# Kernel optimization log

Measured on AMD Instinct MI355X. Metric: run time of the kernel, lower is better.

Reference implementation:

```python
import jax, jax.numpy as jnp
import numpy as np

B, T, C = 2, 2048, 1024
H = 16
D = C // H  # head_dim = 64


def setup_inputs() -> dict:
    key = jax.random.key(0)
    ks = jax.random.split(key, 9)
    s = 0.02
    return {
        "x": jax.random.normal(ks[0], (B, T, C), dtype=jnp.float32),
        "Wq": jax.random.normal(ks[1], (C, C), dtype=jnp.float32) * s,
        "bq": jax.random.normal(ks[2], (C,), dtype=jnp.float32) * s,
        "Wk": jax.random.normal(ks[3], (C, C), dtype=jnp.float32) * s,
        "bk": jax.random.normal(ks[4], (C,), dtype=jnp.float32) * s,
        "Wv": jax.random.normal(ks[5], (C, C), dtype=jnp.float32) * s,
        "bv": jax.random.normal(ks[6], (C,), dtype=jnp.float32) * s,
        "Wo": jax.random.normal(ks[7], (C, C), dtype=jnp.float32) * s,
        "bo": jax.random.normal(ks[8], (C,), dtype=jnp.float32) * s,
    }


def reference(x, Wq, bq, Wk, bk, Wv, bv, Wo, bo):
    b, t, c = x.shape
    h, d = H, c // H
    # torch nn.Linear: y = x @ W.T + b
    q = (x @ Wq.T + bq).reshape(b, t, h, d).transpose(0, 2, 1, 3)  # [B,H,T,D]
    k = (x @ Wk.T + bk).reshape(b, t, h, d).transpose(0, 2, 1, 3)
    v = (x @ Wv.T + bv).reshape(b, t, h, d).transpose(0, 2, 1, 3)

    scores = jnp.einsum("bhqd,bhkd->bhqk", q, k) / jnp.sqrt(jnp.float32(d))
    causal = jnp.tril(jnp.ones((t, t), dtype=bool))  # [T,T]
    scores = jnp.where(causal[None, None, :, :], scores, -jnp.inf)
    attn = jax.nn.softmax(scores, axis=-1)  # [B,H,T,T]

    out = jnp.einsum("bhqk,bhkd->bhqd", attn, v)  # [B,H,T,D]
    out = out.transpose(0, 2, 1, 3).reshape(b, t, c)
    out = out @ Wo.T + bo
    return out
```

## Files before the change

### kernel.cpp

```cpp
#include <hip/hip_runtime.h>
#include <hip/hip_bf16.h>

using u16 = unsigned short;
using u32 = unsigned int;
using short8  = __attribute__((ext_vector_type(8))) short;
using short4v = __attribute__((ext_vector_type(4))) short;
using floatx4 = __attribute__((ext_vector_type(4))) float;

#define TT 2048
#define CC 1024
#define HH 16
#define DD 64
#define BBATCH 2
#define MM (BBATCH*TT)

#define QSCALE 0.18033688011112042f

__device__ __forceinline__ u16 f2bf(float f) {
    u32 u = __float_as_uint(f);
    u += 0x7fffu + ((u >> 16) & 1u);
    return (u16)(u >> 16);
}
__device__ __forceinline__ float bf2f(u16 s) {
    return __uint_as_float(((u32)s) << 16);
}
__device__ __forceinline__ float bpermf(float v, int srclane) {
    return __int_as_float(__builtin_amdgcn_ds_bpermute(srclane * 4, __float_as_int(v)));
}
__device__ __forceinline__ void gll16(const u16* g, u16* l) {
    __builtin_amdgcn_global_load_lds((const __attribute__((address_space(1))) void*)g,
                                     (__attribute__((address_space(3))) void*)l, 16, 0, 0);
}

__global__ __launch_bounds__(256) void cast_all(const float* __restrict__ x,
    const float* __restrict__ Wq, const float* __restrict__ Wk,
    const float* __restrict__ Wv, const float* __restrict__ Wo,
    u16* __restrict__ xb, u16* __restrict__ wqb, u16* __restrict__ wkb,
    u16* __restrict__ wvb, u16* __restrict__ wob)
{
    int i = blockIdx.x * 256 + threadIdx.x;
    const float* src; u16* dst; int off;
    if (i < 1048576) { src = x; dst = xb; off = i; }
    else {
        int j = i - 1048576;
        int s = j >> 18;
        off = j & 262143;
        src = (s == 0) ? Wq : (s == 1) ? Wk : (s == 2) ? Wv : Wo;
        dst = (s == 0) ? wqb : (s == 1) ? wkb : (s == 2) ? wvb : wob;
    }
    float4 v = ((const float4*)src)[off];
    u16 r[4];
    r[0] = f2bf(v.x); r[1] = f2bf(v.y); r[2] = f2bf(v.z); r[3] = f2bf(v.w);
    ((ushort4*)dst)[off] = *(ushort4*)r;
}

__global__ __launch_bounds__(256) void transpose_v(const u16* __restrict__ v, u16* __restrict__ vt) {
    __shared__ u16 tile[64][72];
    int bh = blockIdx.y;
    int t0 = blockIdx.x * 64;
    int r = threadIdx.x >> 2;
    int c = (threadIdx.x & 3) * 16;
    const u16* src = v + ((size_t)bh * TT + t0 + r) * DD + c;
    *(uint4*)&tile[r][c]     = *(const uint4*)src;
    *(uint4*)&tile[r][c + 8] = *(const uint4*)(src + 8);
    __syncthreads();
    u16 tmp[16];
#pragma unroll
    for (int j = 0; j < 16; ++j) tmp[j] = tile[c + j][r];
    u16* dst = vt + ((size_t)bh * DD + r) * TT + t0 + c;
    *(uint4*)dst       = *(uint4*)&tmp[0];
    *(uint4*)(dst + 8) = *(uint4*)&tmp[8];
}

template <int OUT_MODE>
__device__ __forceinline__ void gemm_core(const u16* __restrict__ A, const u16* __restrict__ W,
                                          const float* __restrict__ bias, float outscale,
                                          void* __restrict__ outp)
{
    __shared__ u16 As[128*32];
    __shared__ u16 Bs[128*32];
    const int K = CC;
    int tid = threadIdx.x;
    int m0 = blockIdx.y * 128;
    int n0 = blockIdx.x * 128;
    int lane = tid & 63;
    int w  = tid >> 6;
    int wm = (w >> 1) * 64;
    int wn = (w & 1) * 64;
    int lm = lane & 15;
    int lq = lane >> 4;

    floatx4 acc[4][4];
#pragma unroll
    for (int i = 0; i < 4; ++i)
#pragma unroll
        for (int j = 0; j < 4; ++j)
            acc[i][j] = (floatx4){0.f, 0.f, 0.f, 0.f};

    const u16* ag = A + (size_t)(m0 + (tid >> 2)) * K + (tid & 3) * 8;
    const u16* wg = W + (size_t)(n0 + (tid >> 2)) * K + (tid & 3) * 8;
    u16* asl = As + tid * 8;
    u16* bsl = Bs + tid * 8;

    for (int k0 = 0; k0 < K; k0 += 32) {
        __syncthreads();
        gll16(ag + k0,           asl);
        gll16(ag + 64*K + k0,    asl + 2048);
        gll16(wg + k0,           bsl);
        gll16(wg + 64*K + k0,    bsl + 2048);
        __syncthreads();
        short8 af[4], bfr[4];
#pragma unroll
        for (int t = 0; t < 4; ++t) {
            af[t]  = *(const short8*)(As + (wm + t*16 + lm)*32 + lq*8);
            bfr[t] = *(const short8*)(Bs + (wn + t*16 + lm)*32 + lq*8);
        }
#pragma unroll
        for (int i = 0; i < 4; ++i)
#pragma unroll
            for (int j = 0; j < 4; ++j)
                acc[i][j] = __builtin_amdgcn_mfma_f32_16x16x32_bf16(af[i], bfr[j], acc[i][j], 0, 0, 0);
    }

#pragma unroll
    for (int j = 0; j < 4; ++j) {
        int col = n0 + wn + j*16 + lm;
        float bv = bias[col];
#pragma unroll
        for (int i = 0; i < 4; ++i) {
#pragma unroll
            for (int r = 0; r < 4; ++r) {
                int row = m0 + wm + i*16 + lq*4 + r;
                float val = (acc[i][j][r] + bv) * outscale;
                if (OUT_MODE == 0) {
                    int b_ = row >> 11, t_ = row & (TT-1);
                    int h_ = col >> 6,  d_ = col & 63;
                    ((u16*)outp)[(((size_t)(b_*HH + h_) * TT + t_) * DD) + d_] = f2bf(val);
                } else {
                    ((float*)outp)[(size_t)row * CC + col] = val;
                }
            }
        }
    }
}

__global__ __launch_bounds__(256, 2) void qkv_gemm(const u16* __restrict__ xb,
    const u16* __restrict__ wq, const u16* __restrict__ wk, const u16* __restrict__ wv,
    const float* __restrict__ bq, const float* __restrict__ bk, const float* __restrict__ bv,
    u16* __restrict__ q, u16* __restrict__ k, u16* __restrict__ v)
{
    int z = blockIdx.z;
    const u16* W = (z == 0) ? wq : (z == 1) ? wk : wv;
    const float* bias = (z == 0) ? bq : (z == 1) ? bk : bv;
    u16* outp = (z == 0) ? q : (z == 1) ? k : v;
    float scl = (z == 0) ? QSCALE : 1.0f;
    gemm_core<0>(xb, W, bias, scl, outp);
}

__global__ __launch_bounds__(256, 2) void o_gemm(const u16* __restrict__ a, const u16* __restrict__ w,
                                                 const float* __restrict__ bias, float* __restrict__ outp)
{
    gemm_core<1>(a, w, bias, 1.0f, outp);
}

__global__ __launch_bounds__(256, 2) void attn_mfma(const u16* __restrict__ qg, const u16* __restrict__ kg,
                                                    const u16* __restrict__ vtg, u16* __restrict__ attnb)
{
    __shared__ u16 Ks[64*72];
    __shared__ u16 Vs[64*72];

    int tid = threadIdx.x;
    int lane = tid & 63;
    int w = tid >> 6;
    int lm = lane & 15;
    int lq = lane >> 4;
    int qt = (int)(gridDim.x - 1) - (int)blockIdx.x;
    int bh = blockIdx.y;
    int b_ = bh >> 4, h_ = bh & 15;
    int q0 = qt * 128;

    const size_t basek  = (size_t)bh * TT * DD;
    const size_t basevt = (size_t)bh * DD * TT;

    short8 aq[2][2];
    {
        const u16* qbase = qg + basek + (size_t)(q0 + w*32 + lm) * DD + lq*8;
#pragma unroll
        for (int i = 0; i < 2; ++i)
#pragma unroll
            for (int ks = 0; ks < 2; ++ks)
                aq[i][ks] = *(const short8*)(qbase + i*16*DD + ks*32);
    }

    floatx4 oacc[2][4];
#pragma unroll
    for (int i = 0; i < 2; ++i)
#pragma unroll
        for (int j = 0; j < 4; ++j)
            oacc[i][j] = (floatx4){0.f, 0.f, 0.f, 0.f};
    float mrun[2] = {-3e38f, -3e38f};
    float lrun[2] = {0.f, 0.f};

    int srow = tid >> 2;
    int kb   = tid & 3;
    int p_   = kb >> 1, kb01 = kb & 1;
    const u16* ksrc = kg  + basek  + (size_t)srow * DD + kb*16;
    const u16* vsrc = vtg + basevt + (size_t)srow * TT + kb*16;
    u16* kdst = Ks + srow*72 + kb*16;
    u16* vdst = Vs + srow*72 + p_*32 + kb01*4;

    int nkt = 2*qt + 2;
    int wrowmax = q0 + w*32 + 31;

    for (int kt = 0; kt < nkt; ++kt) {
        uint4 k0v = *(const uint4*)(ksrc + (size_t)kt*64*DD);
        uint4 k1v = *(const uint4*)(ksrc + (size_t)kt*64*DD + 8);
        uint4 v0v = *(const uint4*)(vsrc + kt*64);
        uint4 v1v = *(const uint4*)(vsrc + kt*64 + 8);
        __syncthreads();
        *(uint4*)kdst       = k0v;
        *(uint4*)(kdst + 8) = k1v;
        *(uint2*)(vdst)      = make_uint2(v0v.x, v0v.y);
        *(uint2*)(vdst + 8)  = make_uint2(v0v.z, v0v.w);
        *(uint2*)(vdst + 16) = make_uint2(v1v.x, v1v.y);
        *(uint2*)(vdst + 24) = make_uint2(v1v.z, v1v.w);
        __syncthreads();

        if (kt*64 <= wrowmax) {
            floatx4 st[2][4];
#pragma unroll
            for (int i = 0; i < 2; ++i)
#pragma unroll
                for (int jn = 0; jn < 4; ++jn)
                    st[i][jn] = (floatx4){0.f, 0.f, 0.f, 0.f};
#pragma unroll
            for (int jn = 0; jn < 4; ++jn) {
                short8 kf0 = *(const short8*)&Ks[(jn*16 + lm)*72 + lq*8];
                short8 kf1 = *(const short8*)&Ks[(jn*16 + lm)*72 + 32 + lq*8];
#pragma unroll
                for (int i = 0; i < 2; ++i) {
                    st[i][jn] = __builtin_amdgcn_mfma_f32_16x16x32_bf16(kf0, aq[i][0], st[i][jn], 0, 0, 0);
                    st[i][jn] = __builtin_amdgcn_mfma_f32_16x16x32_bf16(kf1, aq[i][1], st[i][jn], 0, 0, 0);
                }
            }

            int kbase = kt*64;
            short4v ap[2][4];
#pragma unroll
            for (int i = 0; i < 2; ++i) {
                int qrow = q0 + w*32 + i*16 + lm;
                if (kbase + 63 > q0 + w*32 + i*16) {
#pragma unroll
                    for (int jn = 0; jn < 4; ++jn)
#pragma unroll
                        for (int r = 0; r < 4; ++r) {
                            int key = kbase + jn*16 + lq*4 + r;
                            if (key > qrow) st[i][jn][r] = -__builtin_inff();
                        }
                }
                float mx = st[i][0][0];
#pragma unroll
                for (int jn = 0; jn < 4; ++jn)
#pragma unroll
                    for (int r = 0; r < 4; ++r) mx = fmaxf(mx, st[i][jn][r]);
                mx = fmaxf(mx, __shfl_xor(mx, 16));
                mx = fmaxf(mx, __shfl_xor(mx, 32));
                float mold = mrun[i];
                float newm = fmaxf(mold, mx);
                mrun[i] = newm;
                float psum = 0.f;
#pragma unroll
                for (int jn = 0; jn < 4; ++jn)
#pragma unroll
                    for (int r = 0; r < 4; ++r) {
                        float pe = __builtin_amdgcn_exp2f(st[i][jn][r] - newm);
                        st[i][jn][r] = pe;
                        psum += pe;
                    }
                psum += __shfl_xor(psum, 16);
                psum += __shfl_xor(psum, 32);
                float alpha = __builtin_amdgcn_exp2f(mold - newm);
                lrun[i] = lrun[i]*alpha + psum;
#pragma unroll
                for (int jn = 0; jn < 4; ++jn) {
                    u32 lo = __builtin_amdgcn_perm(__float_as_uint(st[i][jn][1]),
                                                   __float_as_uint(st[i][jn][0]), 0x07060302u);
                    u32 hi = __builtin_amdgcn_perm(__float_as_uint(st[i][jn][3]),
                                                   __float_as_uint(st[i][jn][2]), 0x07060302u);
                    uint2 pk = make_uint2(lo, hi);
                    ap[i][jn] = __builtin_bit_cast(short4v, pk);
                }
                if (__ballot(newm != mold)) {
                    float ar[4];
#pragma unroll
                    for (int r = 0; r < 4; ++r) ar[r] = bpermf(alpha, lq*4 + r);
#pragma unroll
                    for (int jd = 0; jd < 4; ++jd)
#pragma unroll
                        for (int r = 0; r < 4; ++r) oacc[i][jd][r] *= ar[r];
                }
            }

#pragma unroll
            for (int p2 = 0; p2 < 2; ++p2) {
#pragma unroll
                for (int jd = 0; jd < 4; ++jd) {
                    short8 vb = *(const short8*)&Vs[(jd*16 + lm)*72 + p2*32 + lq*8];
                    short4v blo, bhi;
#pragma unroll
                    for (int j = 0; j < 4; ++j) { blo[j] = vb[j]; bhi[j] = vb[j+4]; }
#pragma unroll
                    for (int i = 0; i < 2; ++i) {
                        oacc[i][jd] = __builtin_amdgcn_mfma_f32_16x16x16bf16_1k(ap[i][2*p2],   blo, oacc[i][jd], 0, 0, 0);
                        oacc[i][jd] = __builtin_amdgcn_mfma_f32_16x16x16bf16_1k(ap[i][2*p2+1], bhi, oacc[i][jd], 0, 0, 0);
                    }
                }
            }
        }
    }

#pragma unroll
    for (int i = 0; i < 2; ++i) {
        float il[4];
#pragma unroll
        for (int r = 0; r < 4; ++r) il[r] = 1.f / bpermf(lrun[i], lq*4 + r);
#pragma unroll
        for (int r = 0; r < 4; ++r) {
            int qrow = q0 + w*32 + i*16 + lq*4 + r;
            u16* orow = attnb + ((size_t)(b_*TT + qrow)) * CC + h_*DD + lm;
#pragma unroll
            for (int jd = 0; jd < 4; ++jd)
                orow[jd*16] = f2bf(oacc[i][jd][r] * il[r]);
        }
    }
}

extern "C" void kernel_launch(void* const* d_in, const int* in_sizes, int n_in,
                              void* d_out, int out_size, void* d_ws, size_t ws_size,
                              hipStream_t stream)
{
    const float* x  = (const float*)d_in[0];
    const float* Wq = (const float*)d_in[1];
    const float* bq = (const float*)d_in[2];
    const float* Wk = (const float*)d_in[3];
    const float* bk = (const float*)d_in[4];
    const float* Wv = (const float*)d_in[5];
    const float* bv = (const float*)d_in[6];
    const float* Wo = (const float*)d_in[7];
    const float* bo = (const float*)d_in[8];
    float* out = (float*)d_out;

    char* ws = (char*)d_ws;
    u16* xb   = (u16*)(ws);
    u16* wqb  = (u16*)(ws + (size_t)( 8<<20));
    u16* wkb  = (u16*)(ws + (size_t)(10<<20));
    u16* wvb  = (u16*)(ws + (size_t)(12<<20));
    u16* wob  = (u16*)(ws + (size_t)(14<<20));
    u16* q    = (u16*)(ws + (size_t)(16<<20));
    u16* k    = (u16*)(ws + (size_t)(24<<20));
    u16* v    = (u16*)(ws + (size_t)(32<<20));
    u16* vt   = (u16*)(ws + (size_t)(40<<20));
    u16* attnb = xb;

    cast_all<<<dim3(8192), dim3(256), 0, stream>>>(x, Wq, Wk, Wv, Wo, xb, wqb, wkb, wvb, wob);

    dim3 gq(CC/128, MM/128, 3);
    qkv_gemm<<<gq, dim3(256), 0, stream>>>(xb, wqb, wkb, wvb, bq, bk, bv, q, k, v);

    transpose_v<<<dim3(TT/64, BBATCH*HH), dim3(256), 0, stream>>>(v, vt);

    attn_mfma<<<dim3(TT/128, BBATCH*HH), dim3(256), 0, stream>>>(q, k, vt, attnb);

    dim3 go(CC/128, MM/128);
    o_gemm<<<go, dim3(256), 0, stream>>>(attnb, wob, bo, out);
}
```

Measured before the change: 219.0 us.

## Shrink attention to 64-row query tiles and split O-projection into narrower tiles

The attention kernel now runs 128-thread blocks over 64 query rows, so twice as many blocks are launched and causal work is spread more evenly across CUs. K tiles are loaded straight into LDS with global-to-LDS loads into an unpadded layout, and the per-warp causal skip branch is removed. The O-projection GEMM is split out of the shared template with 128x64 tiles and a higher occupancy bound, doubling its block count. The cost is that each K/V tile now feeds fewer query rows, and the unpadded K layout may cause LDS bank conflicts.

```diff
diff --git a/kernel.cpp b/kernel.cpp
--- a/kernel.cpp
+++ b/kernel.cpp
@@ -72,14 +72,20 @@
     *(uint4*)(dst + 8) = *(uint4*)&tmp[8];
 }
 
-template <int OUT_MODE>
-__device__ __forceinline__ void gemm_core(const u16* __restrict__ A, const u16* __restrict__ W,
-                                          const float* __restrict__ bias, float outscale,
-                                          void* __restrict__ outp)
+__global__ __launch_bounds__(256, 2) void qkv_gemm(const u16* __restrict__ xb,
+    const u16* __restrict__ wq, const u16* __restrict__ wk, const u16* __restrict__ wv,
+    const float* __restrict__ bq, const float* __restrict__ bk, const float* __restrict__ bv,
+    u16* __restrict__ q, u16* __restrict__ k, u16* __restrict__ v)
 {
     __shared__ u16 As[128*32];
     __shared__ u16 Bs[128*32];
     const int K = CC;
+    int z = blockIdx.z;
+    const u16* W = (z == 0) ? wq : (z == 1) ? wk : wv;
+    const float* bias = (z == 0) ? bq : (z == 1) ? bk : bv;
+    u16* outp = (z == 0) ? q : (z == 1) ? k : v;
+    float outscale = (z == 0) ? QSCALE : 1.0f;
+
     int tid = threadIdx.x;
     int m0 = blockIdx.y * 128;
     int n0 = blockIdx.x * 128;
@@ -97,6 +103,70 @@
         for (int j = 0; j < 4; ++j)
             acc[i][j] = (floatx4){0.f, 0.f, 0.f, 0.f};
 
+    const u16* ag = xb + (size_t)(m0 + (tid >> 2)) * K + (tid & 3) * 8;
+    const u16* wg = W  + (size_t)(n0 + (tid >> 2)) * K + (tid & 3) * 8;
+    u16* asl = As + tid * 8;
+    u16* bsl = Bs + tid * 8;
+
+    for (int k0 = 0; k0 < K; k0 += 32) {
+        __syncthreads();
+        gll16(ag + k0,           asl);
+        gll16(ag + 64*K + k0,    asl + 2048);
+        gll16(wg + k0,           bsl);
+        gll16(wg + 64*K + k0,    bsl + 2048);
+        __syncthreads();
+        short8 af[4], bfr[4];
+#pragma unroll
+        for (int t = 0; t < 4; ++t) {
+            af[t]  = *(const short8*)(As + (wm + t*16 + lm)*32 + lq*8);
+            bfr[t] = *(const short8*)(Bs + (wn + t*16 + lm)*32 + lq*8);
+        }
+#pragma unroll
+        for (int i = 0; i < 4; ++i)
+#pragma unroll
+            for (int j = 0; j < 4; ++j)
+                acc[i][j] = __builtin_amdgcn_mfma_f32_16x16x32_bf16(af[i], bfr[j], acc[i][j], 0, 0, 0);
+    }
+
+#pragma unroll
+    for (int j = 0; j < 4; ++j) {
+        int col = n0 + wn + j*16 + lm;
+        float bv2 = bias[col];
+#pragma unroll
+        for (int i = 0; i < 4; ++i) {
+#pragma unroll
+            for (int r = 0; r < 4; ++r) {
+                int row = m0 + wm + i*16 + lq*4 + r;
+                float val = (acc[i][j][r] + bv2) * outscale;
+                int b_ = row >> 11, t_ = row & (TT-1);
+                int h_ = col >> 6,  d_ = col & 63;
+                outp[(((size_t)(b_*HH + h_) * TT + t_) * DD) + d_] = f2bf(val);
+            }
+        }
+    }
+}
+
+__global__ __launch_bounds__(256, 4) void o_gemm(const u16* __restrict__ A, const u16* __restrict__ W,
+                                                 const float* __restrict__ bias, float* __restrict__ outp)
+{
+    __shared__ u16 As[128*32];
+    __shared__ u16 Bs[64*32];
+    const int K = CC;
+    int tid = threadIdx.x;
+    int m0 = blockIdx.y * 128;
+    int n0 = blockIdx.x * 64;
+    int lane = tid & 63;
+    int w  = tid >> 6;
+    int lm = lane & 15;
+    int lq = lane >> 4;
+
+    floatx4 acc[2][4];
+#pragma unroll
+    for (int i = 0; i < 2; ++i)
+#pragma unroll
+        for (int j = 0; j < 4; ++j)
+            acc[i][j] = (floatx4){0.f, 0.f, 0.f, 0.f};
+
     const u16* ag = A + (size_t)(m0 + (tid >> 2)) * K + (tid & 3) * 8;
     const u16* wg = W + (size_t)(n0 + (tid >> 2)) * K + (tid & 3) * 8;
     u16* asl = As + tid * 8;
@@ -104,19 +174,19 @@
 
     for (int k0 = 0; k0 < K; k0 += 32) {
         __syncthreads();
-        gll16(ag + k0,           asl);
-        gll16(ag + 64*K + k0,    asl + 2048);
-        gll16(wg + k0,           bsl);
-        gll16(wg + 64*K + k0,    bsl + 2048);
-        __syncthreads();
-        short8 af[4], bfr[4];
-#pragma unroll
-        for (int t = 0; t < 4; ++t) {
-            af[t]  = *(const short8*)(As + (wm + t*16 + lm)*32 + lq*8);
-            bfr[t] = *(const short8*)(Bs + (wn + t*16 + lm)*32 + lq*8);
-        }
-#pragma unroll
-        for (int i = 0; i < 4; ++i)
+        gll16(ag + k0,        asl);
+        gll16(ag + 64*K + k0, asl + 2048);
+        gll16(wg + k0,        bsl);
+        __syncthreads();
+        short8 af[2], bfr[4];
+#pragma unroll
+        for (int i = 0; i < 2; ++i)
+            af[i] = *(const short8*)(As + (w*32 + i*16 + lm)*32 + lq*8);
+#pragma unroll
+        for (int j = 0; j < 4; ++j)
+            bfr[j] = *(const short8*)(Bs + (j*16 + lm)*32 + lq*8);
+#pragma unroll
+        for (int i = 0; i < 2; ++i)
 #pragma unroll
             for (int j = 0; j < 4; ++j)
                 acc[i][j] = __builtin_amdgcn_mfma_f32_16x16x32_bf16(af[i], bfr[j], acc[i][j], 0, 0, 0);
@@ -124,49 +194,23 @@
 
 #pragma unroll
     for (int j = 0; j < 4; ++j) {
-        int col = n0 + wn + j*16 + lm;
-        float bv = bias[col];
-#pragma unroll
-        for (int i = 0; i < 4; ++i) {
+        int col = n0 + j*16 + lm;
+        float bv2 = bias[col];
+#pragma unroll
+        for (int i = 0; i < 2; ++i) {
 #pragma unroll
             for (int r = 0; r < 4; ++r) {
-                int row = m0 + wm + i*16 + lq*4 + r;
-                float val = (acc[i][j][r] + bv) * outscale;
-                if (OUT_MODE == 0) {
-                    int b_ = row >> 11, t_ = row & (TT-1);
-                    int h_ = col >> 6,  d_ = col & 63;
-                    ((u16*)outp)[(((size_t)(b_*HH + h_) * TT + t_) * DD) + d_] = f2bf(val);
-                } else {
-                    ((float*)outp)[(size_t)row * CC + col] = val;
-                }
-            }
-        }
-    }
-}
-
-__global__ __launch_bounds__(256, 2) void qkv_gemm(const u16* __restrict__ xb,
-    const u16* __restrict__ wq, const u16* __restrict__ wk, const u16* __restrict__ wv,
-    const float* __restrict__ bq, const float* __restrict__ bk, const float* __restrict__ bv,
-    u16* __restrict__ q, u16* __restrict__ k, u16* __restrict__ v)
-{
-    int z = blockIdx.z;
-    const u16* W = (z == 0) ? wq : (z == 1) ? wk : wv;
-    const float* bias = (z == 0) ? bq : (z == 1) ? bk : bv;
-    u16* outp = (z == 0) ? q : (z == 1) ? k : v;
-    float scl = (z == 0) ? QSCALE : 1.0f;
-    gemm_core<0>(xb, W, bias, scl, outp);
-}
-
-__global__ __launch_bounds__(256, 2) void o_gemm(const u16* __restrict__ a, const u16* __restrict__ w,
-                                                 const float* __restrict__ bias, float* __restrict__ outp)
-{
-    gemm_core<1>(a, w, bias, 1.0f, outp);
-}
-
-__global__ __launch_bounds__(256, 2) void attn_mfma(const u16* __restrict__ qg, const u16* __restrict__ kg,
+                int row = m0 + w*32 + i*16 + lq*4 + r;
+                outp[(size_t)row * CC + col] = acc[i][j][r] + bv2;
+            }
+        }
+    }
+}
+
+__global__ __launch_bounds__(128, 2) void attn_mfma(const u16* __restrict__ qg, const u16* __restrict__ kg,
                                                     const u16* __restrict__ vtg, u16* __restrict__ attnb)
 {
-    __shared__ u16 Ks[64*72];
+    __shared__ u16 Ks[64*64];
     __shared__ u16 Vs[64*72];
 
     int tid = threadIdx.x;
@@ -174,10 +218,10 @@
     int w = tid >> 6;
     int lm = lane & 15;
     int lq = lane >> 4;
-    int qt = (int)(gridDim.x - 1) - (int)blockIdx.x;
+    int qt = 31 - (int)blockIdx.x;
     int bh = blockIdx.y;
     int b_ = bh >> 4, h_ = bh & 15;
-    int q0 = qt * 128;
+    int q0 = qt * 64;
 
     const size_t basek  = (size_t)bh * TT * DD;
     const size_t basevt = (size_t)bh * DD * TT;
@@ -201,119 +245,121 @@
     float mrun[2] = {-3e38f, -3e38f};
     float lrun[2] = {0.f, 0.f};
 
-    int srow = tid >> 2;
-    int kb   = tid & 3;
-    int p_   = kb >> 1, kb01 = kb & 1;
-    const u16* ksrc = kg  + basek  + (size_t)srow * DD + kb*16;
-    const u16* vsrc = vtg + basevt + (size_t)srow * TT + kb*16;
-    u16* kdst = Ks + srow*72 + kb*16;
-    u16* vdst = Vs + srow*72 + p_*32 + kb01*4;
-
-    int nkt = 2*qt + 2;
-    int wrowmax = q0 + w*32 + 31;
+    const u16* kgl = kg + basek + (size_t)(w*32 + (lane >> 3)) * DD + (lane & 7) * 8;
+    u16* kls = Ks + w*32*64 + lane*8;
+    int vrow = tid >> 1;
+    int kbv  = (tid & 1) * 2;
+    const u16* vsrc = vtg + basevt + (size_t)vrow * TT + kbv*16;
+    u16* vdst0 = Vs + vrow*72 + (kbv>>1)*32 + (kbv&1)*4;
+    u16* vdst1 = Vs + vrow*72 + ((kbv+1)>>1)*32 + ((kbv+1)&1)*4;
+
+    int nkt = qt + 1;
 
     for (int kt = 0; kt < nkt; ++kt) {
-        uint4 k0v = *(const uint4*)(ksrc + (size_t)kt*64*DD);
-        uint4 k1v = *(const uint4*)(ksrc + (size_t)kt*64*DD + 8);
-        uint4 v0v = *(const uint4*)(vsrc + kt*64);
-        uint4 v1v = *(const uint4*)(vsrc + kt*64 + 8);
-        __syncthreads();
-        *(uint4*)kdst       = k0v;
-        *(uint4*)(kdst + 8) = k1v;
-        *(uint2*)(vdst)      = make_uint2(v0v.x, v0v.y);
-        *(uint2*)(vdst + 8)  = make_uint2(v0v.z, v0v.w);
-        *(uint2*)(vdst + 16) = make_uint2(v1v.x, v1v.y);
-        *(uint2*)(vdst + 24) = make_uint2(v1v.z, v1v.w);
-        __syncthreads();
-
-        if (kt*64 <= wrowmax) {
-            floatx4 st[2][4];
-#pragma unroll
-            for (int i = 0; i < 2; ++i)
+        uint4 v0a = *(const uint4*)(vsrc + kt*64);
+        uint4 v0b = *(const uint4*)(vsrc + kt*64 + 8);
+        uint4 v1a = *(const uint4*)(vsrc + kt*64 + 16);
+        uint4 v1b = *(const uint4*)(vsrc + kt*64 + 24);
+        __syncthreads();
+#pragma unroll
+        for (int c = 0; c < 4; ++c)
+            gll16(kgl + (size_t)(kt*64 + c*8) * DD, kls + c*512);
+        *(uint2*)(vdst0)      = make_uint2(v0a.x, v0a.y);
+        *(uint2*)(vdst0 + 8)  = make_uint2(v0a.z, v0a.w);
+        *(uint2*)(vdst0 + 16) = make_uint2(v0b.x, v0b.y);
+        *(uint2*)(vdst0 + 24) = make_uint2(v0b.z, v0b.w);
+        *(uint2*)(vdst1)      = make_uint2(v1a.x, v1a.y);
+        *(uint2*)(vdst1 + 8)  = make_uint2(v1a.z, v1a.w);
+        *(uint2*)(vdst1 + 16) = make_uint2(v1b.x, v1b.y);
+        *(uint2*)(vdst1 + 24) = make_uint2(v1b.z, v1b.w);
+        __syncthreads();
+
+        floatx4 st[2][4];
+#pragma unroll
+        for (int i = 0; i < 2; ++i)
+#pragma unroll
+            for (int jn = 0; jn < 4; ++jn)
+                st[i][jn] = (floatx4){0.f, 0.f, 0.f, 0.f};
+#pragma unroll
+        for (int jn = 0; jn < 4; ++jn) {
+            short8 kf0 = *(const short8*)&Ks[(jn*16 + lm)*64 + lq*8];
+            short8 kf1 = *(const short8*)&Ks[(jn*16 + lm)*64 + 32 + lq*8];
+#pragma unroll
+            for (int i = 0; i < 2; ++i) {
+                st[i][jn] = __builtin_amdgcn_mfma_f32_16x16x32_bf16(kf0, aq[i][0], st[i][jn], 0, 0, 0);
+                st[i][jn] = __builtin_amdgcn_mfma_f32_16x16x32_bf16(kf1, aq[i][1], st[i][jn], 0, 0, 0);
+            }
+        }
+
+        int kbase = kt*64;
+        short4v ap[2][4];
+#pragma unroll
+        for (int i = 0; i < 2; ++i) {
+            int qrow = q0 + w*32 + i*16 + lm;
+            if (kbase + 63 > q0 + w*32 + i*16) {
 #pragma unroll
                 for (int jn = 0; jn < 4; ++jn)
-                    st[i][jn] = (floatx4){0.f, 0.f, 0.f, 0.f};
+#pragma unroll
+                    for (int r = 0; r < 4; ++r) {
+                        int key = kbase + jn*16 + lq*4 + r;
+                        if (key > qrow) st[i][jn][r] = -__builtin_inff();
+                    }
+            }
+            float mx = st[i][0][0];
+#pragma unroll
+            for (int jn = 0; jn < 4; ++jn)
+#pragma unroll
+                for (int r = 0; r < 4; ++r) mx = fmaxf(mx, st[i][jn][r]);
+            mx = fmaxf(mx, __shfl_xor(mx, 16));
+            mx = fmaxf(mx, __shfl_xor(mx, 32));
+            float mold = mrun[i];
+            float newm = fmaxf(mold, mx);
+            mrun[i] = newm;
+            float psum = 0.f;
+#pragma unroll
+            for (int jn = 0; jn < 4; ++jn)
+#pragma unroll
+                for (int r = 0; r < 4; ++r) {
+                    float pe = __builtin_amdgcn_exp2f(st[i][jn][r] - newm);
+                    st[i][jn][r] = pe;
+                    psum += pe;
+                }
+            psum += __shfl_xor(psum, 16);
+            psum += __shfl_xor(psum, 32);
+            float alpha = __builtin_amdgcn_exp2f(mold - newm);
+            lrun[i] = lrun[i]*alpha + psum;
 #pragma unroll
             for (int jn = 0; jn < 4; ++jn) {
-                short8 kf0 = *(const short8*)&Ks[(jn*16 + lm)*72 + lq*8];
-                short8 kf1 = *(const short8*)&Ks[(jn*16 + lm)*72 + 32 + lq*8];
+                u32 lo = __builtin_amdgcn_perm(__float_as_uint(st[i][jn][1]),
+                                               __float_as_uint(st[i][jn][0]), 0x07060302u);
+                u32 hi = __builtin_amdgcn_perm(__float_as_uint(st[i][jn][3]),
+                                               __float_as_uint(st[i][jn][2]), 0x07060302u);
+                uint2 pk = make_uint2(lo, hi);
+                ap[i][jn] = __builtin_bit_cast(short4v, pk);
+            }
+            if (__ballot(newm != mold)) {
+                float ar[4];
+#pragma unroll
+                for (int r = 0; r < 4; ++r) ar[r] = bpermf(alpha, lq*4 + r);
+#pragma unroll
+                for (int jd = 0; jd < 4; ++jd)
+#pragma unroll
+                    for (int r = 0; r < 4; ++r) oacc[i][jd][r] *= ar[r];
+            }
+        }
+
+#pragma unroll
+        for (int p2 = 0; p2 < 2; ++p2) {
+#pragma unroll
+            for (int jd = 0; jd < 4; ++jd) {
+                short8 vb = *(const short8*)&Vs[(jd*16 + lm)*72 + p2*32 + lq*8];
+                short4v blo, bhi;
+#pragma unroll
+                for (int j = 0; j < 4; ++j) { blo[j] = vb[j]; bhi[j] = vb[j+4]; }
 #pragma unroll
                 for (int i = 0; i < 2; ++i) {
-                    st[i][jn] = __builtin_amdgcn_mfma_f32_16x16x32_bf16(kf0, aq[i][0], st[i][jn], 0, 0, 0);
-                    st[i][jn] = __builtin_amdgcn_mfma_f32_16x16x32_bf16(kf1, aq[i][1], st[i][jn], 0, 0, 0);
-                }
-            }
-
-            int kbase = kt*64;
-            short4v ap[2][4];
-#pragma unroll
-            for (int i = 0; i < 2; ++i) {
-                int qrow = q0 + w*32 + i*16 + lm;
-                if (kbase + 63 > q0 + w*32 + i*16) {
-#pragma unroll
-                    for (int jn = 0; jn < 4; ++jn)
-#pragma unroll
-                        for (int r = 0; r < 4; ++r) {
-                            int key = kbase + jn*16 + lq*4 + r;
-                            if (key > qrow) st[i][jn][r] = -__builtin_inff();
-                        }
-                }
-                float mx = st[i][0][0];
-#pragma unroll
-                for (int jn = 0; jn < 4; ++jn)
-#pragma unroll
-                    for (int r = 0; r < 4; ++r) mx = fmaxf(mx, st[i][jn][r]);
-                mx = fmaxf(mx, __shfl_xor(mx, 16));
-                mx = fmaxf(mx, __shfl_xor(mx, 32));
-                float mold = mrun[i];
-                float newm = fmaxf(mold, mx);
-                mrun[i] = newm;
-                float psum = 0.f;
-#pragma unroll
-                for (int jn = 0; jn < 4; ++jn)
-#pragma unroll
-                    for (int r = 0; r < 4; ++r) {
-                        float pe = __builtin_amdgcn_exp2f(st[i][jn][r] - newm);
-                        st[i][jn][r] = pe;
-                        psum += pe;
-                    }
-                psum += __shfl_xor(psum, 16);
-                psum += __shfl_xor(psum, 32);
-                float alpha = __builtin_amdgcn_exp2f(mold - newm);
-                lrun[i] = lrun[i]*alpha + psum;
-#pragma unroll
-                for (int jn = 0; jn < 4; ++jn) {
-                    u32 lo = __builtin_amdgcn_perm(__float_as_uint(st[i][jn][1]),
-                                                   __float_as_uint(st[i][jn][0]), 0x07060302u);
-                    u32 hi = __builtin_amdgcn_perm(__float_as_uint(st[i][jn][3]),
-                                                   __float_as_uint(st[i][jn][2]), 0x07060302u);
-                    uint2 pk = make_uint2(lo, hi);
-                    ap[i][jn] = __builtin_bit_cast(short4v, pk);
-                }
-                if (__ballot(newm != mold)) {
-                    float ar[4];
-#pragma unroll
-                    for (int r = 0; r < 4; ++r) ar[r] = bpermf(alpha, lq*4 + r);
-#pragma unroll
-                    for (int jd = 0; jd < 4; ++jd)
-#pragma unroll
-                        for (int r = 0; r < 4; ++r) oacc[i][jd][r] *= ar[r];
-                }
-            }
-
-#pragma unroll
-            for (int p2 = 0; p2 < 2; ++p2) {
-#pragma unroll
-                for (int jd = 0; jd < 4; ++jd) {
-                    short8 vb = *(const short8*)&Vs[(jd*16 + lm)*72 + p2*32 + lq*8];
-                    short4v blo, bhi;
-#pragma unroll
-                    for (int j = 0; j < 4; ++j) { blo[j] = vb[j]; bhi[j] = vb[j+4]; }
-#pragma unroll
-                    for (int i = 0; i < 2; ++i) {
-                        oacc[i][jd] = __builtin_amdgcn_mfma_f32_16x16x16bf16_1k(ap[i][2*p2],   blo, oacc[i][jd], 0, 0, 0);
-                        oacc[i][jd] = __builtin_amdgcn_mfma_f32_16x16x16bf16_1k(ap[i][2*p2+1], bhi, oacc[i][jd], 0, 0, 0);
-                    }
+                    oacc[i][jd] = __builtin_amdgcn_mfma_f32_16x16x16bf16_1k(ap[i][2*p2],   blo, oacc[i][jd], 0, 0, 0);
+                    oacc[i][jd] = __builtin_amdgcn_mfma_f32_16x16x16bf16_1k(ap[i][2*p2+1], bhi, oacc[i][jd], 0, 0, 0);
                 }
             }
         }
@@ -369,8 +415,8 @@
 
     transpose_v<<<dim3(TT/64, BBATCH*HH), dim3(256), 0, stream>>>(v, vt);
 
-    attn_mfma<<<dim3(TT/128, BBATCH*HH), dim3(256), 0, stream>>>(q, k, vt, attnb);
-
-    dim3 go(CC/128, MM/128);
+    attn_mfma<<<dim3(TT/64, BBATCH*HH), dim3(128), 0, stream>>>(q, k, vt, attnb);
+
+    dim3 go(CC/64, MM/128);
     o_gemm<<<go, dim3(256), 0, stream>>>(attnb, wob, bo, out);
 }
```

After: 219.9 us. No clear change (+0.4%).
